# Performance work log

Hardware: AMD Instinct MI355X
Metric: run time of the kernel (lower is better)

Reference implementation:

```python
import jax, jax.numpy as jnp
import numpy as np

jax.config.update("jax_enable_x64", True)  # needed for faithful float64 bit reinterpretation

VOCAB = 50257
HIDDEN = 1024
MAX_POS = 4096
TYPE_VOCAB = 2
NUM_FEATS = 94
PROJ_INTER = 256
NUM_TOKEN_ID = 5
LN_EPS = 1e-12


def _layer_norm(x, g, b, eps=LN_EPS):
    mu = jnp.mean(x, axis=-1, keepdims=True)
    var = jnp.var(x, axis=-1, keepdims=True)
    return (x - mu) * jax.lax.rsqrt(var + eps) * g + b


def _numeric_features(values, formats):
    # values: [B,S] float32 (torch casts to float64 internally), formats: [B,S] int
    v = values.astype(jnp.float64)
    # float64_binary_repr (64 bits). Torch: (int64_view & (1<<i)) > 0; bit 63 mask
    # overflows to INT64_MIN so (x & mask) > 0 is always False -> replicate exactly.
    bits = jax.lax.bitcast_convert_type(v, jnp.int64)
    masks = jnp.left_shift(jnp.int64(1), jnp.arange(64, dtype=jnp.int64))
    binary = ((bits[..., None] & masks) > 0).astype(jnp.float32)  # [B,S,64]
    av = jnp.abs(v)
    fl = jnp.floor(av)
    units = jnp.clip(fl % 10.0, 0, 9).astype(jnp.int32)
    oh_units = jax.nn.one_hot(units, 10, dtype=jnp.float32)       # [B,S,10]
    tens = jnp.clip((fl // 10.0) % 10.0, 0, 9).astype(jnp.int32)
    oh_tens = jax.nn.one_hot(tens, 10, dtype=jnp.float32)         # [B,S,10]
    log_v = jnp.log(av + 1e-6).astype(jnp.float32)
    sign = jnp.sign(v).astype(jnp.float32)
    expo = jnp.where(av > 1e-6, jnp.floor(jnp.log10(jnp.maximum(av, 1e-300))), 0.0).astype(jnp.float32)
    is_int = (av == fl).astype(jnp.float32)
    is_pos = (v > 0).astype(jnp.float32)
    is_zero = (v == 0.0).astype(jnp.float32)
    is_neg = (v < 0).astype(jnp.float32)
    pos_int = (v == jnp.floor(v)) & (v > 0)
    l2 = jnp.log2(jnp.maximum(v, 1.0))
    is_pow2 = (pos_int & (l2 == jnp.floor(l2))).astype(jnp.float32)
    fmt_int = (formats == 0).astype(jnp.float32)
    fmt_float = (formats == 1).astype(jnp.float32)
    scalars = jnp.stack([log_v, sign, expo, is_int, is_pos, is_zero, is_neg, is_pow2, fmt_int, fmt_float], axis=-1)
    return jnp.concatenate([binary, oh_units, oh_tens, scalars], axis=-1)  # [B,S,94]


def setup_inputs() -> dict:
    key = jax.random.key(0)
    ks = jax.random.split(key, 12)
    B, S = 8, 2048
    input_ids = jax.random.randint(ks[0], (B, S), 0, VOCAB, dtype=jnp.int64)
    numeric_values = jax.random.normal(ks[1], (B, S), dtype=jnp.float32) * 100.0
    numeric_formats = jax.random.randint(ks[2], (B, S), 0, 2, dtype=jnp.int64)
    s = 0.02
    W_word = (jax.random.normal(ks[3], (VOCAB, HIDDEN), dtype=jnp.float32) * s).at[0].set(0.0)  # padding_idx=0
    W_pos = jax.random.normal(ks[4], (MAX_POS, HIDDEN), dtype=jnp.float32) * s
    W_type = jax.random.normal(ks[5], (TYPE_VOCAB, HIDDEN), dtype=jnp.float32) * s
    ln_g = jnp.ones((HIDDEN,), jnp.float32)
    ln_b = jnp.zeros((HIDDEN,), jnp.float32)
    p_w1 = jax.random.normal(ks[6], (NUM_FEATS, PROJ_INTER), dtype=jnp.float32) * s
    p_b1 = jnp.zeros((PROJ_INTER,), jnp.float32)
    p_w2 = jax.random.normal(ks[7], (PROJ_INTER, HIDDEN), dtype=jnp.float32) * s
    p_b2 = jnp.zeros((HIDDEN,), jnp.float32)
    pln_g = jnp.ones((HIDDEN,), jnp.float32)
    pln_b = jnp.zeros((HIDDEN,), jnp.float32)
    return dict(input_ids=input_ids, numeric_values=numeric_values, numeric_formats=numeric_formats,
                W_word=W_word, W_pos=W_pos, W_type=W_type, ln_g=ln_g, ln_b=ln_b,
                p_w1=p_w1, p_b1=p_b1, p_w2=p_w2, p_b2=p_b2, pln_g=pln_g, pln_b=pln_b)


def reference(input_ids, numeric_values, numeric_formats, W_word, W_pos, W_type,
              ln_g, ln_b, p_w1, p_b1, p_w2, p_b2, pln_g, pln_b):
    B, S = input_ids.shape
    # text embeddings: word + position + token_type (token_type_ids default = 0)
    text = W_word[input_ids] + W_pos[jnp.arange(S)][None, :, :] + W_type[0][None, None, :]
    text = text.astype(jnp.float32)
    # active numeric positions: [NUM] token AND non-NaN value
    active = (input_ids == NUM_TOKEN_ID) & ~jnp.isnan(numeric_values)  # [B,S]
    safe_vals = jnp.where(active, numeric_values, 1.0)
    feats = _numeric_features(safe_vals, numeric_formats)  # [B,S,94] float32
    # numeric projection MLP: Linear -> GELU -> Linear -> LayerNorm
    h = jax.nn.gelu(feats @ p_w1 + p_b1, approximate=False)
    num_emb = _layer_norm(h @ p_w2 + p_b2, pln_g, pln_b)
    num_emb = jnp.where(active[..., None], num_emb, 0.0)  # scatter into zeros
    # fusion_type == 'add', then final LayerNorm (dropout p=0 -> identity)
    out = _layer_norm(text + num_emb, ln_g, ln_b)
    return out
```

## Files before the change

kernel.cpp:

```cpp
#include <hip/hip_runtime.h>
#include <math.h>

#define HIDDEN 1024
#define SEQ 2048
#define NF 94
#define PI 256
#define NUM_TOKEN 5

__device__ __forceinline__ void block_sum2(float& a, float& b, float* scr, int tid) {
    #pragma unroll
    for (int off = 32; off > 0; off >>= 1) {
        a += __shfl_down(a, off, 64);
        b += __shfl_down(b, off, 64);
    }
    const int lane = tid & 63, wv = tid >> 6;
    __syncthreads();
    if (lane == 0) { scr[wv] = a; scr[4 + wv] = b; }
    __syncthreads();
    a = scr[0] + scr[1] + scr[2] + scr[3];
    b = scr[4] + scr[5] + scr[6] + scr[7];
}

__global__ __launch_bounds__(256)
void blackhole_emb_kernel(const int* __restrict__ ids,
                          const float* __restrict__ vals,
                          const int* __restrict__ fmts,
                          const float* __restrict__ Ww,
                          const float* __restrict__ Wp,
                          const float* __restrict__ Wt,
                          const float* __restrict__ lng,
                          const float* __restrict__ lnb,
                          const float* __restrict__ w1,
                          const float* __restrict__ b1,
                          const float* __restrict__ w2,
                          const float* __restrict__ b2,
                          const float* __restrict__ plng,
                          const float* __restrict__ plnb,
                          float* __restrict__ out)
{
    __shared__ float sh_feats[NF];
    __shared__ float sh_h[PI];
    __shared__ float sh_num[HIDDEN];
    __shared__ float scr[8];

    const int token = blockIdx.x;
    const int s     = token & (SEQ - 1);
    const int tid   = threadIdx.x;

    const int   id   = ids[token];
    const float vraw = vals[token];
    const bool active = (id == NUM_TOKEN) && !isnan(vraw);

    const float4 aw = ((const float4*)(Ww + (size_t)id * HIDDEN))[tid];
    const float4 ap = ((const float4*)(Wp + (size_t)s  * HIDDEN))[tid];
    const float4 at = ((const float4*)Wt)[tid];
    float x[4] = { aw.x + ap.x + at.x, aw.y + ap.y + at.y,
                   aw.z + ap.z + at.z, aw.w + ap.w + at.w };

    if (active) {
        const double    v    = (double)vraw;
        const double    av   = fabs(v);
        const long long bits = __double_as_longlong(v);
        const double    fl   = floor(av);
        const int       fmt  = fmts[token];

        if (tid < NF) {
            float f;
            if (tid < 64) {
                f = (tid < 63 && ((bits >> tid) & 1LL)) ? 1.0f : 0.0f;
            } else if (tid < 74) {
                const int units = (int)fmin(fmax(fmod(fl, 10.0), 0.0), 9.0);
                f = (tid - 64 == units) ? 1.0f : 0.0f;
            } else if (tid < 84) {
                const int tens = (int)fmin(fmax(fmod(floor(fl / 10.0), 10.0), 0.0), 9.0);
                f = (tid - 74 == tens) ? 1.0f : 0.0f;
            } else {
                switch (tid - 84) {
                    case 0: f = (float)log(av + 1e-6); break;
                    case 1: f = (v > 0.0) ? 1.0f : ((v < 0.0) ? -1.0f : 0.0f); break;
                    case 2: f = (av > 1e-6) ? (float)floor(log10(fmax(av, 1e-300))) : 0.0f; break;
                    case 3: f = (av == fl) ? 1.0f : 0.0f; break;
                    case 4: f = (v > 0.0) ? 1.0f : 0.0f; break;
                    case 5: f = (v == 0.0) ? 1.0f : 0.0f; break;
                    case 6: f = (v < 0.0) ? 1.0f : 0.0f; break;
                    case 7: {
                        const bool   pos_int = (v == floor(v)) && (v > 0.0);
                        const double l2      = log2(fmax(v, 1.0));
                        f = (pos_int && (l2 == floor(l2))) ? 1.0f : 0.0f;
                        break;
                    }
                    case 8:  f = (fmt == 0) ? 1.0f : 0.0f; break;
                    default: f = (fmt == 1) ? 1.0f : 0.0f; break;
                }
            }
            sh_feats[tid] = f;
        }
        __syncthreads();

        float acc = b1[tid];
        #pragma unroll 2
        for (int k = 0; k < NF; ++k)
            acc = fmaf(sh_feats[k], w1[k * PI + tid], acc);
        acc = 0.5f * acc * (1.0f + erff(acc * 0.70710678118654752f));
        sh_h[tid] = acc;
        __syncthreads();

        float n0 = b2[tid], n1 = b2[tid + 256], n2 = b2[tid + 512], n3 = b2[tid + 768];
        for (int k = 0; k < PI; ++k) {
            const float  hk = sh_h[k];
            const float* r  = w2 + (size_t)k * HIDDEN;
            n0 = fmaf(hk, r[tid],       n0);
            n1 = fmaf(hk, r[tid + 256], n1);
            n2 = fmaf(hk, r[tid + 512], n2);
            n3 = fmaf(hk, r[tid + 768], n3);
        }

        float sm = n0 + n1 + n2 + n3;
        float sq = n0*n0 + n1*n1 + n2*n2 + n3*n3;
        block_sum2(sm, sq, scr, tid);
        const float mu   = sm * (1.0f / HIDDEN);
        const float var  = sq * (1.0f / HIDDEN) - mu * mu;
        const float rstd = rsqrtf(var + 1e-12f);
        sh_num[tid      ] = (n0 - mu) * rstd * plng[tid      ] + plnb[tid      ];
        sh_num[tid + 256] = (n1 - mu) * rstd * plng[tid + 256] + plnb[tid + 256];
        sh_num[tid + 512] = (n2 - mu) * rstd * plng[tid + 512] + plnb[tid + 512];
        sh_num[tid + 768] = (n3 - mu) * rstd * plng[tid + 768] + plnb[tid + 768];
        __syncthreads();

        x[0] += sh_num[tid * 4 + 0];
        x[1] += sh_num[tid * 4 + 1];
        x[2] += sh_num[tid * 4 + 2];
        x[3] += sh_num[tid * 4 + 3];
    }

    float sm = x[0] + x[1] + x[2] + x[3];
    float sq = x[0]*x[0] + x[1]*x[1] + x[2]*x[2] + x[3]*x[3];
    block_sum2(sm, sq, scr, tid);
    const float mu   = sm * (1.0f / HIDDEN);
    const float var  = sq * (1.0f / HIDDEN) - mu * mu;
    const float rstd = rsqrtf(var + 1e-12f);

    const float4 g4 = ((const float4*)lng)[tid];
    const float4 b4 = ((const float4*)lnb)[tid];
    float4 o;
    o.x = (x[0] - mu) * rstd * g4.x + b4.x;
    o.y = (x[1] - mu) * rstd * g4.y + b4.y;
    o.z = (x[2] - mu) * rstd * g4.z + b4.z;
    o.w = (x[3] - mu) * rstd * g4.w + b4.w;
    ((float4*)(out + (size_t)token * HIDDEN))[tid] = o;
}

extern "C" void kernel_launch(void* const* d_in, const int* in_sizes, int n_in,
                              void* d_out, int out_size, void* d_ws, size_t ws_size,
                              hipStream_t stream) {
    const int*   ids  = (const int*)d_in[0];
    const float* vals = (const float*)d_in[1];
    const int*   fmts = (const int*)d_in[2];
    const float* Ww   = (const float*)d_in[3];
    const float* Wp   = (const float*)d_in[4];
    const float* Wt   = (const float*)d_in[5];
    const float* lng  = (const float*)d_in[6];
    const float* lnb  = (const float*)d_in[7];
    const float* w1   = (const float*)d_in[8];
    const float* b1   = (const float*)d_in[9];
    const float* w2   = (const float*)d_in[10];
    const float* b2   = (const float*)d_in[11];
    const float* plng = (const float*)d_in[12];
    const float* plnb = (const float*)d_in[13];
    float* out = (float*)d_out;

    const int tokens = in_sizes[0];
    blackhole_emb_kernel<<<tokens, 256, 0, stream>>>(
        ids, vals, fmts, Ww, Wp, Wt, lng, lnb, w1, b1, w2, b2, plng, plnb, out);
}
```

Measured before the change: 307.7 us.

## Map one token per wavefront and replace block reductions with wave shuffles

Each 256-thread block now handles four tokens, one per 64-lane wavefront, instead of one token per block. Features, the MLP and both layer norms are computed inside the wave with shuffle broadcasts and xor reductions, which removes shared memory and __syncthreads. Output writes use nontemporal stores. The trade-off is that active (numeric) tokens now run the full MLP on a single wave, so divergence between the waves of a block can leave lanes idle.

```diff
diff --git a/kernel.cpp b/kernel.cpp
--- a/kernel.cpp
+++ b/kernel.cpp
@@ -7,18 +7,10 @@
 #define PI 256
 #define NUM_TOKEN 5
 
-__device__ __forceinline__ void block_sum2(float& a, float& b, float* scr, int tid) {
-    #pragma unroll
-    for (int off = 32; off > 0; off >>= 1) {
-        a += __shfl_down(a, off, 64);
-        b += __shfl_down(b, off, 64);
-    }
-    const int lane = tid & 63, wv = tid >> 6;
-    __syncthreads();
-    if (lane == 0) { scr[wv] = a; scr[4 + wv] = b; }
-    __syncthreads();
-    a = scr[0] + scr[1] + scr[2] + scr[3];
-    b = scr[4] + scr[5] + scr[6] + scr[7];
+typedef float vfloat4 __attribute__((ext_vector_type(4)));
+
+__device__ __forceinline__ float gelu_exact(float a) {
+    return 0.5f * a * (1.0f + erff(a * 0.70710678118654752f));
 }
 
 __global__ __launch_bounds__(256)
@@ -36,26 +28,35 @@
                           const float* __restrict__ b2,
                           const float* __restrict__ plng,
                           const float* __restrict__ plnb,
-                          float* __restrict__ out)
+                          float* __restrict__ out,
+                          int tokens)
 {
-    __shared__ float sh_feats[NF];
-    __shared__ float sh_h[PI];
-    __shared__ float sh_num[HIDDEN];
-    __shared__ float scr[8];
-
-    const int token = blockIdx.x;
-    const int s     = token & (SEQ - 1);
-    const int tid   = threadIdx.x;
-
-    const int   id   = ids[token];
-    const float vraw = vals[token];
-    const bool active = (id == NUM_TOKEN) && !isnan(vraw);
-
-    const float4 aw = ((const float4*)(Ww + (size_t)id * HIDDEN))[tid];
-    const float4 ap = ((const float4*)(Wp + (size_t)s  * HIDDEN))[tid];
-    const float4 at = ((const float4*)Wt)[tid];
-    float x[4] = { aw.x + ap.x + at.x, aw.y + ap.y + at.y,
-                   aw.z + ap.z + at.z, aw.w + ap.w + at.w };
+    const int lane  = threadIdx.x & 63;
+    const int wv    = threadIdx.x >> 6;
+    const int token = blockIdx.x * 4 + wv;
+    if (token >= tokens) return;
+    const int s = token & (SEQ - 1);
+
+    const int   id     = ids[token];
+    const float vraw   = vals[token];
+    const bool  active = (id == NUM_TOKEN) && !isnan(vraw);
+
+    const float* wrow = Ww + (size_t)id * HIDDEN;
+    const float* prow = Wp + (size_t)s  * HIDDEN;
+    const int    col0 = lane * 4;
+
+    float x[4][4];
+    #pragma unroll
+    for (int j = 0; j < 4; ++j) {
+        const int off = j * 256 + col0;
+        const float4 aw = *(const float4*)(wrow + off);
+        const float4 ap = *(const float4*)(prow + off);
+        const float4 at = *(const float4*)(Wt   + off);
+        x[j][0] = aw.x + ap.x + at.x;
+        x[j][1] = aw.y + ap.y + at.y;
+        x[j][2] = aw.z + ap.z + at.z;
+        x[j][3] = aw.w + ap.w + at.w;
+    }
 
     if (active) {
         const double    v    = (double)vraw;
@@ -64,90 +65,128 @@
         const double    fl   = floor(av);
         const int       fmt  = fmts[token];
 
-        if (tid < NF) {
-            float f;
-            if (tid < 64) {
-                f = (tid < 63 && ((bits >> tid) & 1LL)) ? 1.0f : 0.0f;
-            } else if (tid < 74) {
-                const int units = (int)fmin(fmax(fmod(fl, 10.0), 0.0), 9.0);
-                f = (tid - 64 == units) ? 1.0f : 0.0f;
-            } else if (tid < 84) {
-                const int tens = (int)fmin(fmax(fmod(floor(fl / 10.0), 10.0), 0.0), 9.0);
-                f = (tid - 74 == tens) ? 1.0f : 0.0f;
-            } else {
-                switch (tid - 84) {
-                    case 0: f = (float)log(av + 1e-6); break;
-                    case 1: f = (v > 0.0) ? 1.0f : ((v < 0.0) ? -1.0f : 0.0f); break;
-                    case 2: f = (av > 1e-6) ? (float)floor(log10(fmax(av, 1e-300))) : 0.0f; break;
-                    case 3: f = (av == fl) ? 1.0f : 0.0f; break;
-                    case 4: f = (v > 0.0) ? 1.0f : 0.0f; break;
-                    case 5: f = (v == 0.0) ? 1.0f : 0.0f; break;
-                    case 6: f = (v < 0.0) ? 1.0f : 0.0f; break;
-                    case 7: {
-                        const bool   pos_int = (v == floor(v)) && (v > 0.0);
-                        const double l2      = log2(fmax(v, 1.0));
-                        f = (pos_int && (l2 == floor(l2))) ? 1.0f : 0.0f;
-                        break;
-                    }
-                    case 8:  f = (fmt == 0) ? 1.0f : 0.0f; break;
-                    default: f = (fmt == 1) ? 1.0f : 0.0f; break;
+        float f0 = (lane < 63 && ((bits >> lane) & 1LL)) ? 1.0f : 0.0f;
+        float f1 = 0.0f;
+        if (lane < 10) {
+            const int units = (int)fmin(fmax(fmod(fl, 10.0), 0.0), 9.0);
+            f1 = (lane == units) ? 1.0f : 0.0f;
+        } else if (lane < 20) {
+            const int tens = (int)fmin(fmax(fmod(floor(fl / 10.0), 10.0), 0.0), 9.0);
+            f1 = (lane - 10 == tens) ? 1.0f : 0.0f;
+        } else if (lane < 30) {
+            switch (lane - 20) {
+                case 0: f1 = (float)log(av + 1e-6); break;
+                case 1: f1 = (v > 0.0) ? 1.0f : ((v < 0.0) ? -1.0f : 0.0f); break;
+                case 2: f1 = (av > 1e-6) ? (float)floor(log10(fmax(av, 1e-300))) : 0.0f; break;
+                case 3: f1 = (av == fl) ? 1.0f : 0.0f; break;
+                case 4: f1 = (v > 0.0) ? 1.0f : 0.0f; break;
+                case 5: f1 = (v == 0.0) ? 1.0f : 0.0f; break;
+                case 6: f1 = (v < 0.0) ? 1.0f : 0.0f; break;
+                case 7: {
+                    const bool   pos_int = (v == floor(v)) && (v > 0.0);
+                    const double l2      = log2(fmax(v, 1.0));
+                    f1 = (pos_int && (l2 == floor(l2))) ? 1.0f : 0.0f;
+                    break;
+                }
+                case 8: f1 = (fmt == 0) ? 1.0f : 0.0f; break;
+                case 9: f1 = (fmt == 1) ? 1.0f : 0.0f; break;
+            }
+        }
+
+        float acc[4] = { b1[lane], b1[lane + 64], b1[lane + 128], b1[lane + 192] };
+        for (int k = 0; k < 64; ++k) {
+            const float  fk  = __shfl(f0, k, 64);
+            const float* col = w1 + k * PI;
+            acc[0] = fmaf(fk, col[lane],       acc[0]);
+            acc[1] = fmaf(fk, col[lane + 64],  acc[1]);
+            acc[2] = fmaf(fk, col[lane + 128], acc[2]);
+            acc[3] = fmaf(fk, col[lane + 192], acc[3]);
+        }
+        for (int k = 0; k < NF - 64; ++k) {
+            const float  fk  = __shfl(f1, k, 64);
+            const float* col = w1 + (64 + k) * PI;
+            acc[0] = fmaf(fk, col[lane],       acc[0]);
+            acc[1] = fmaf(fk, col[lane + 64],  acc[1]);
+            acc[2] = fmaf(fk, col[lane + 128], acc[2]);
+            acc[3] = fmaf(fk, col[lane + 192], acc[3]);
+        }
+        float h[4];
+        #pragma unroll
+        for (int i = 0; i < 4; ++i) h[i] = gelu_exact(acc[i]);
+
+        float n[4][4];
+        #pragma unroll
+        for (int j = 0; j < 4; ++j) {
+            const float4 bb = *(const float4*)(b2 + j * 256 + col0);
+            n[j][0] = bb.x; n[j][1] = bb.y; n[j][2] = bb.z; n[j][3] = bb.w;
+        }
+        #pragma unroll
+        for (int i = 0; i < 4; ++i) {
+            for (int kk = 0; kk < 64; ++kk) {
+                const float  hk  = __shfl(h[i], kk, 64);
+                const float* row = w2 + (size_t)(i * 64 + kk) * HIDDEN;
+                #pragma unroll
+                for (int j = 0; j < 4; ++j) {
+                    const float4 w = *(const float4*)(row + j * 256 + col0);
+                    n[j][0] = fmaf(hk, w.x, n[j][0]);
+                    n[j][1] = fmaf(hk, w.y, n[j][1]);
+                    n[j][2] = fmaf(hk, w.z, n[j][2]);
+                    n[j][3] = fmaf(hk, w.w, n[j][3]);
                 }
             }
-            sh_feats[tid] = f;
-        }
-        __syncthreads();
-
-        float acc = b1[tid];
-        #pragma unroll 2
-        for (int k = 0; k < NF; ++k)
-            acc = fmaf(sh_feats[k], w1[k * PI + tid], acc);
-        acc = 0.5f * acc * (1.0f + erff(acc * 0.70710678118654752f));
-        sh_h[tid] = acc;
-        __syncthreads();
-
-        float n0 = b2[tid], n1 = b2[tid + 256], n2 = b2[tid + 512], n3 = b2[tid + 768];
-        for (int k = 0; k < PI; ++k) {
-            const float  hk = sh_h[k];
-            const float* r  = w2 + (size_t)k * HIDDEN;
-            n0 = fmaf(hk, r[tid],       n0);
-            n1 = fmaf(hk, r[tid + 256], n1);
-            n2 = fmaf(hk, r[tid + 512], n2);
-            n3 = fmaf(hk, r[tid + 768], n3);
-        }
-
-        float sm = n0 + n1 + n2 + n3;
-        float sq = n0*n0 + n1*n1 + n2*n2 + n3*n3;
-        block_sum2(sm, sq, scr, tid);
+        }
+
+        float sm = 0.0f, sq = 0.0f;
+        #pragma unroll
+        for (int j = 0; j < 4; ++j)
+            #pragma unroll
+            for (int c = 0; c < 4; ++c) { sm += n[j][c]; sq += n[j][c] * n[j][c]; }
+        #pragma unroll
+        for (int off = 32; off > 0; off >>= 1) {
+            sm += __shfl_xor(sm, off, 64);
+            sq += __shfl_xor(sq, off, 64);
+        }
         const float mu   = sm * (1.0f / HIDDEN);
         const float var  = sq * (1.0f / HIDDEN) - mu * mu;
         const float rstd = rsqrtf(var + 1e-12f);
-        sh_num[tid      ] = (n0 - mu) * rstd * plng[tid      ] + plnb[tid      ];
-        sh_num[tid + 256] = (n1 - mu) * rstd * plng[tid + 256] + plnb[tid + 256];
-        sh_num[tid + 512] = (n2 - mu) * rstd * plng[tid + 512] + plnb[tid + 512];
-        sh_num[tid + 768] = (n3 - mu) * rstd * plng[tid + 768] + plnb[tid + 768];
-        __syncthreads();
-
-        x[0] += sh_num[tid * 4 + 0];
-        x[1] += sh_num[tid * 4 + 1];
-        x[2] += sh_num[tid * 4 + 2];
-        x[3] += sh_num[tid * 4 + 3];
-    }
-
-    float sm = x[0] + x[1] + x[2] + x[3];
-    float sq = x[0]*x[0] + x[1]*x[1] + x[2]*x[2] + x[3]*x[3];
-    block_sum2(sm, sq, scr, tid);
+        #pragma unroll
+        for (int j = 0; j < 4; ++j) {
+            const float4 g4 = *(const float4*)(plng + j * 256 + col0);
+            const float4 b4 = *(const float4*)(plnb + j * 256 + col0);
+            x[j][0] += (n[j][0] - mu) * rstd * g4.x + b4.x;
+            x[j][1] += (n[j][1] - mu) * rstd * g4.y + b4.y;
+            x[j][2] += (n[j][2] - mu) * rstd * g4.z + b4.z;
+            x[j][3] += (n[j][3] - mu) * rstd * g4.w + b4.w;
+        }
+    }
+
+    float sm = 0.0f, sq = 0.0f;
+    #pragma unroll
+    for (int j = 0; j < 4; ++j)
+        #pragma unroll
+        for (int c = 0; c < 4; ++c) { sm += x[j][c]; sq += x[j][c] * x[j][c]; }
+    #pragma unroll
+    for (int off = 32; off > 0; off >>= 1) {
+        sm += __shfl_xor(sm, off, 64);
+        sq += __shfl_xor(sq, off, 64);
+    }
     const float mu   = sm * (1.0f / HIDDEN);
     const float var  = sq * (1.0f / HIDDEN) - mu * mu;
     const float rstd = rsqrtf(var + 1e-12f);
 
-    const float4 g4 = ((const float4*)lng)[tid];
-    const float4 b4 = ((const float4*)lnb)[tid];
-    float4 o;
-    o.x = (x[0] - mu) * rstd * g4.x + b4.x;
-    o.y = (x[1] - mu) * rstd * g4.y + b4.y;
-    o.z = (x[2] - mu) * rstd * g4.z + b4.z;
-    o.w = (x[3] - mu) * rstd * g4.w + b4.w;
-    ((float4*)(out + (size_t)token * HIDDEN))[tid] = o;
+    float* orow = out + (size_t)token * HIDDEN;
+    #pragma unroll
+    for (int j = 0; j < 4; ++j) {
+        const int off = j * 256 + col0;
+        const float4 g4 = *(const float4*)(lng + off);
+        const float4 b4 = *(const float4*)(lnb + off);
+        vfloat4 o;
+        o.x = (x[j][0] - mu) * rstd * g4.x + b4.x;
+        o.y = (x[j][1] - mu) * rstd * g4.y + b4.y;
+        o.z = (x[j][2] - mu) * rstd * g4.z + b4.z;
+        o.w = (x[j][3] - mu) * rstd * g4.w + b4.w;
+        __builtin_nontemporal_store(o, (vfloat4*)(orow + off));
+    }
 }
 
 extern "C" void kernel_launch(void* const* d_in, const int* in_sizes, int n_in,
@@ -170,6 +209,7 @@
     float* out = (float*)d_out;
 
     const int tokens = in_sizes[0];
-    blackhole_emb_kernel<<<tokens, 256, 0, stream>>>(
-        ids, vals, fmts, Ww, Wp, Wt, lng, lnb, w1, b1, w2, b2, plng, plnb, out);
+    const int blocks = (tokens + 3) / 4;
+    blackhole_emb_kernel<<<blocks, 256, 0, stream>>>(
+        ids, vals, fmts, Ww, Wp, Wt, lng, lnb, w1, b1, w2, b2, plng, plnb, out, tokens);
 }
```

After: 304.5 us. About the same (-1.0%).
